# Performance work log

Hardware: AMD Instinct MI355X
Metric: run time of the kernel (lower is better)

Reference implementation:

```python
import math
import jax, jax.numpy as jnp
import numpy as np

B, IMG, CIN = 32, 32, 4
PATCH, HIDDEN, DEPTH, HEADS, MLP = 2, 768, 12, 12, 3072
FREQ, NUM_CLASSES = 256, 1000
GRID = IMG // PATCH
N = GRID * GRID
OUT = PATCH * PATCH * CIN


def _pos_embed(dim, length):
    # faithful port of get_2d_sincos_pos_embed
    g = int(math.sqrt(length))
    grid = np.stack(np.meshgrid(np.arange(g, dtype=np.float32),
                                np.arange(g, dtype=np.float32), indexing='ij')).reshape(2, -1)
    def emb1d(d, pos):
        omega = 1.0 / 10000.0 ** (np.arange(d // 2, dtype=np.float32) / (d / 2.0))
        out = np.einsum('m,d->md', pos, omega)
        return np.concatenate([np.sin(out), np.cos(out)], axis=1)
    pe = np.concatenate([emb1d(dim // 2, grid[0]), emb1d(dim // 2, grid[1])], axis=1)
    return jnp.asarray(pe[None], dtype=jnp.float32)  # [1, N, dim]


def _ln(x):
    # LayerNorm(elementwise_affine=False), eps=1e-5, biased variance
    m = jnp.mean(x, axis=-1, keepdims=True)
    v = jnp.var(x, axis=-1, keepdims=True)
    return (x - m) * jax.lax.rsqrt(v + 1e-5)


def setup_inputs() -> dict:
    key = jax.random.key(0)
    ks = jax.random.split(key, 20)
    w = lambda k, shape: jax.random.normal(k, shape, jnp.float32) * 0.02
    z = lambda *shape: jnp.zeros(shape, jnp.float32)
    return {
        'x': jax.random.normal(ks[0], (B, IMG, IMG, CIN), jnp.float32),
        't': jax.random.uniform(ks[1], (B,), jnp.float32) * 1000.0,
        'y': jax.random.randint(ks[2], (B,), 0, NUM_CLASSES + 1),
        'patch_w': w(ks[3], (PATCH * PATCH * CIN, HIDDEN)), 'patch_b': z(HIDDEN),
        't_w1': w(ks[4], (FREQ, HIDDEN)), 't_b1': z(HIDDEN),
        't_w2': w(ks[5], (HIDDEN, HIDDEN)), 't_b2': z(HIDDEN),
        'label_emb': w(ks[6], (NUM_CLASSES + 1, HIDDEN)),
        'ada_w': w(ks[7], (DEPTH, HIDDEN, 6 * HIDDEN)), 'ada_b': z(DEPTH, 6 * HIDDEN),
        'q_w': w(ks[8], (DEPTH, HIDDEN, HIDDEN)), 'q_b': z(DEPTH, HIDDEN),
        'k_w': w(ks[9], (DEPTH, HIDDEN, HIDDEN)), 'k_b': z(DEPTH, HIDDEN),
        'v_w': w(ks[10], (DEPTH, HIDDEN, HIDDEN)), 'v_b': z(DEPTH, HIDDEN),
        'o_w': w(ks[11], (DEPTH, HIDDEN, HIDDEN)), 'o_b': z(DEPTH, HIDDEN),
        'fc1_w': w(ks[12], (DEPTH, HIDDEN, MLP)), 'fc1_b': z(DEPTH, MLP),
        'fc2_w': w(ks[13], (DEPTH, MLP, HIDDEN)), 'fc2_b': z(DEPTH, HIDDEN),
        'fin_ada_w': w(ks[14], (HIDDEN, 2 * HIDDEN)), 'fin_ada_b': z(2 * HIDDEN),
        'fin_w': w(ks[15], (HIDDEN, OUT)), 'fin_b': z(OUT),
    }


def reference(x, t, y, patch_w, patch_b, t_w1, t_b1, t_w2, t_b2, label_emb,
              ada_w, ada_b, q_w, q_b, k_w, k_b, v_w, v_b, o_w, o_b,
              fc1_w, fc1_b, fc2_w, fc2_b, fin_ada_w, fin_ada_b, fin_w, fin_b):
    Bx = x.shape[0]
    dh = HIDDEN // HEADS
    # patch embed (conv k=p, stride=p == per-patch linear)
    patches = x.reshape(Bx, GRID, PATCH, GRID, PATCH, CIN)
    patches = patches.transpose(0, 1, 3, 2, 4, 5).reshape(Bx, N, PATCH * PATCH * CIN)
    h = patches @ patch_w + patch_b + _pos_embed(HIDDEN, N)
    # timestep embedding: [cos, sin] order
    half = FREQ // 2
    freqs = jnp.exp(-math.log(10000.0) * jnp.arange(half, dtype=jnp.float32) / half)
    args = t.astype(jnp.float32)[:, None] * freqs[None]
    temb = jnp.concatenate([jnp.cos(args), jnp.sin(args)], axis=-1)
    temb = jax.nn.silu(temb @ t_w1 + t_b1) @ t_w2 + t_b2
    c_act = jax.nn.silu(temb + label_emb[y])  # silu applied inside each block on c

    def block(hx, p):
        aw, ab, qw, qb, kw, kb, vw, vb, ow, ob, f1w, f1b, f2w, f2b = p
        ada = c_act @ aw + ab
        sh_m, sc_m, g_m, sh_p, sc_p, g_p = jnp.split(ada, 6, axis=-1)
        xn = _ln(hx) * (1.0 + sc_m[:, None]) + sh_m[:, None]
        q = ((xn @ qw + qb).reshape(Bx, N, HEADS, dh)) / math.sqrt(3.0)
        k = (xn @ kw + kb).reshape(Bx, N, HEADS, dh)
        v = (xn @ vw + vb).reshape(Bx, N, HEADS, dh)
        attn = jax.nn.softmax(jnp.einsum('bqhc,bkhc->bhqk', q, k).astype(jnp.float32), axis=-1)
        yv = jnp.einsum('bhqk,bkhc->bqhc', attn, v).reshape(Bx, N, HIDDEN)
        hx = hx + g_m[:, None] * (yv @ ow + ob)
        xn2 = _ln(hx) * (1.0 + sc_p[:, None]) + sh_p[:, None]
        mlp = jax.nn.gelu(xn2 @ f1w + f1b, approximate=False) @ f2w + f2b
        hx = hx + g_p[:, None] * mlp
        return hx, None

    h, _ = jax.lax.scan(block, h, (ada_w, ada_b, q_w, q_b, k_w, k_b, v_w, v_b,
                                   o_w, o_b, fc1_w, fc1_b, fc2_w, fc2_b))
    # final layer
    fada = c_act @ fin_ada_w + fin_ada_b
    sh, sc = jnp.split(fada, 2, axis=-1)
    out = (_ln(h) * (1.0 + sc[:, None]) + sh[:, None]) @ fin_w + fin_b
    return out  # [B, N, patch*patch*out_channels]
```

## Files before the change

### kernel.cpp

```cpp
#include <hip/hip_runtime.h>
#include <hip/hip_bf16.h>


typedef short  s16x8 __attribute__((ext_vector_type(8)));
typedef float  f32x4 __attribute__((ext_vector_type(4)));

__device__ __forceinline__ float bf2f(unsigned short u) {
    union { unsigned int i; float f; } v; v.i = ((unsigned int)u) << 16; return v.f;
}
__device__ __forceinline__ unsigned short f2bf(float f) {
    union { float f; unsigned int i; } v; v.f = f;
    unsigned int r = (v.i + 0x7FFFu + ((v.i >> 16) & 1u)) >> 16;
    return (unsigned short)r;
}
__device__ __forceinline__ float silu(float v) { return v / (1.f + __expf(-v)); }

__device__ __forceinline__ void gload16(const void* gptr, void* lptr) {
    __builtin_amdgcn_global_load_lds(
        (const __attribute__((address_space(1))) unsigned int*)gptr,
        (__attribute__((address_space(3))) unsigned int*)lptr,
        16, 0, 0);
}

#define ROWS 8192
#define HID  768
#define MLPD 3072
#define ADA_LD 4608

__global__ __launch_bounds__(256) void ada_init(const float* __restrict__ ada_b,
                                                const float* __restrict__ fada_b,
                                                const float* __restrict__ t_b1,
                                                const float* __restrict__ t_b2,
                                                const float* __restrict__ lemb,
                                                const int* __restrict__ y,
                                                float* __restrict__ ada_all,
                                                float* __restrict__ fada,
                                                float* __restrict__ z1,
                                                float* __restrict__ z2)
{
    const int bid = blockIdx.x, tid = threadIdx.x;
    if (bid >= 222) {
        const int col = (bid - 222) * 256 + tid;
        const float b1v = t_b1[col], b2v = t_b2[col];
        for (int r = 0; r < 32; ++r) {
            z1[(size_t)r * HID + col] = b1v;
            z2[(size_t)r * HID + col] = b2v + lemb[(size_t)y[r] * HID + col];
        }
        return;
    }
    const float* Bv; float* Out; int ldw, colb;
    if (bid < 216) {
        const int l = bid / 18; colb = (bid % 18) * 256;
        Bv = ada_b + (size_t)l * ADA_LD; Out = ada_all + (size_t)l * 32 * ADA_LD; ldw = ADA_LD;
    } else {
        colb = (bid - 216) * 256;
        Bv = fada_b; Out = fada; ldw = 1536;
    }
    const int col = colb + tid;
    const float bb = Bv[col];
    #pragma unroll
    for (int r = 0; r < 32; ++r) Out[(size_t)r * ldw + col] = bb;
}

__global__ __launch_bounds__(256) void temb1_k(const float* __restrict__ t,
                                               const float* __restrict__ w1,
                                               float* __restrict__ z1)
{
    __shared__ float tin[128];
    const int b = blockIdx.x, cc = blockIdx.y, kc = blockIdx.z, tid = threadIdx.x;
    const int k0 = kc * 128;
    if (tid < 128) {
        const int k = k0 + tid, j = k & 127;
        const float fr = __expf((float)j * (-9.210340371976184f / 128.f));
        const float a = t[b] * fr;
        tin[tid] = (k < 128) ? cosf(a) : sinf(a);
    }
    __syncthreads();
    const int col = cc * 256 + tid;
    float acc = 0.f;
    #pragma unroll 8
    for (int kk = 0; kk < 128; ++kk) acc += tin[kk] * w1[(size_t)(k0 + kk) * HID + col];
    atomicAdd(&z1[(size_t)b * HID + col], acc);
}

__global__ __launch_bounds__(256) void temb2_k(const float* __restrict__ z1,
                                               const float* __restrict__ w2,
                                               float* __restrict__ z2)
{
    __shared__ float tin[192];
    const int b = blockIdx.x, cc = blockIdx.y, kc = blockIdx.z, tid = threadIdx.x;
    const int k0 = kc * 192;
    if (tid < 192) tin[tid] = silu(z1[(size_t)b * HID + k0 + tid]);
    __syncthreads();
    const int col = cc * 256 + tid;
    float acc = 0.f;
    #pragma unroll 8
    for (int kk = 0; kk < 192; ++kk) acc += tin[kk] * w2[(size_t)(k0 + kk) * HID + col];
    atomicAdd(&z2[(size_t)b * HID + col], acc);
}

__global__ __launch_bounds__(256) void ada_gemm2(const float* __restrict__ z2,
                                                 const float* __restrict__ ada_w,
                                                 const float* __restrict__ fada_w,
                                                 float* __restrict__ ada_all,
                                                 float* __restrict__ fada)
{
    const int bx = blockIdx.x, kc = blockIdx.y, tid = threadIdx.x;
    const float* W; float* Out; int ldw, colb;
    if (bx < 216) {
        const int l = bx / 18; colb = (bx % 18) * 256;
        W = ada_w + (size_t)l * HID * ADA_LD; Out = ada_all + (size_t)l * 32 * ADA_LD; ldw = ADA_LD;
    } else {
        colb = (bx - 216) * 256;
        W = fada_w; Out = fada; ldw = 1536;
    }
    const int col = colb + tid;
    const int k0 = kc * 96;
    __shared__ float cs_[32][96];
    for (int i = tid; i < 32 * 96; i += 256)
        cs_[i / 96][i % 96] = silu(z2[(size_t)(i / 96) * HID + k0 + (i % 96)]);
    __syncthreads();
    float acc[32];
    #pragma unroll
    for (int r = 0; r < 32; ++r) acc[r] = 0.f;
    #pragma unroll 2
    for (int kk = 0; kk < 96; kk += 4) {
        const float w0 = W[(size_t)(k0 + kk) * ldw + col];
        const float w1 = W[(size_t)(k0 + kk + 1) * ldw + col];
        const float w2 = W[(size_t)(k0 + kk + 2) * ldw + col];
        const float w3 = W[(size_t)(k0 + kk + 3) * ldw + col];
        #pragma unroll
        for (int r = 0; r < 32; ++r) {
            const float4 cv = *(const float4*)&cs_[r][kk];
            acc[r] += cv.x * w0 + cv.y * w1 + cv.z * w2 + cv.w * w3;
        }
    }
    #pragma unroll
    for (int r = 0; r < 32; ++r) atomicAdd(&Out[(size_t)r * ldw + col], acc[r]);
}

__global__ __launch_bounds__(256) void patch_embed(const float* __restrict__ x,
                                                   const float* __restrict__ pw,
                                                   const float* __restrict__ pb,
                                                   float* __restrict__ h)
{
    const int row = blockIdx.x;
    const int b = row >> 8, n = row & 255;
    const int gi = n >> 4, gj = n & 15;
    const int tid = threadIdx.x;
    __shared__ float pv[16];
    if (tid < 16) {
        const int pr = tid >> 3, pc = (tid >> 2) & 1, ci = tid & 3;
        pv[tid] = x[((size_t)(b * 32 + gi * 2 + pr) * 32 + (gj * 2 + pc)) * 4 + ci];
    }
    __syncthreads();
    #pragma unroll
    for (int cc = 0; cc < 3; ++cc) {
        const int col = cc * 256 + tid;
        float acc = pb[col];
        #pragma unroll
        for (int i = 0; i < 16; ++i) acc += pv[i] * pw[(size_t)i * HID + col];
        const int d4 = (col < 384) ? col : col - 384;
        const int pos = (col < 384) ? gi : gj;
        const float kf = (float)(d4 < 192 ? d4 : d4 - 192);
        const float om = __expf(kf * (-9.210340371976184f / 192.f));
        const float a = (float)pos * om;
        acc += (d4 < 192) ? sinf(a) : cosf(a);
        h[(size_t)row * HID + col] = acc;
    }
}

__global__ __launch_bounds__(256) void convert_weights(
    const float* __restrict__ q_w, const float* __restrict__ k_w,
    const float* __restrict__ v_w, const float* __restrict__ o_w,
    const float* __restrict__ fc1_w, const float* __restrict__ fc2_w,
    const float* __restrict__ q_b, const float* __restrict__ k_b,
    const float* __restrict__ v_b,
    unsigned short* __restrict__ wbase, size_t slot_stride,
    float* __restrict__ cbias, int first_layer)
{
    const int bid = blockIdx.x;
    const int l = first_layer + bid / 6913;
    const int t = bid % 6913;
    unsigned short* dst = wbase + (size_t)(bid / 6913) * slot_stride;
    const int tid = threadIdx.x;
    if (t == 6912) {
        float* cb = cbias + (size_t)l * 2304;
        for (int i = tid; i < 2304; i += 256) {
            float v;
            if (i < 768)       v = q_b[(size_t)l * 768 + i];
            else if (i < 1536) v = k_b[(size_t)l * 768 + i - 768];
            else               v = v_b[(size_t)l * 768 + i - 1536];
            cb[i] = v;
        }
        return;
    }
    const float* src; int srcN; unsigned short* d; int dLd; int tr, tc;
    if (t < 2304) {
        const int mat = t / 576, tt = t % 576; tr = tt / 24; tc = tt % 24;
        srcN = 768; dLd = 768;
        if (mat == 0)      { src = q_w + (size_t)l * 589824; d = dst; }
        else if (mat == 1) { src = k_w + (size_t)l * 589824; d = dst + 589824; }
        else if (mat == 2) { src = v_w + (size_t)l * 589824; d = dst + 1179648; }
        else               { src = o_w + (size_t)l * 589824; d = dst + 1769472; }
    } else if (t < 4608) {
        const int tt = t - 2304; tr = tt / 96; tc = tt % 96;
        src = fc1_w + (size_t)l * 2359296; srcN = 3072; dLd = 768; d = dst + 2359296;
    } else {
        const int tt = t - 4608; tr = tt / 24; tc = tt % 24;
        src = fc2_w + (size_t)l * 2359296; srcN = 768; dLd = 3072; d = dst + 4718592;
    }
    __shared__ float lt[32][33];
    const int tx = tid & 31, ty = tid >> 5;
    const int r0 = tr * 32, c0 = tc * 32;
    #pragma unroll
    for (int i = 0; i < 4; ++i)
        lt[ty + i * 8][tx] = src[(size_t)(r0 + ty + i * 8) * srcN + c0 + tx];
    __syncthreads();
    const int q = tid & 15;
    const int cw = tid >> 4;
    #pragma unroll
    for (int i = 0; i < 2; ++i) {
        const int cc = cw + i * 16;
        const unsigned int pk = (unsigned int)f2bf(lt[2 * q][cc])
                              | ((unsigned int)f2bf(lt[2 * q + 1][cc]) << 16);
        *(unsigned int*)&d[(size_t)(c0 + cc) * dLd + r0 + 2 * q] = pk;
    }
}

__global__ __launch_bounds__(192) void ln_mod(const float* __restrict__ hbuf,
                                              const float* __restrict__ mod,
                                              int sh_off, int sc_off, int mld,
                                              unsigned short* __restrict__ xout)
{
    const int row = blockIdx.x, tid = threadIdx.x;
    const float4 xv = *(const float4*)&hbuf[(size_t)row * HID + tid * 4];
    float s = (xv.x + xv.y) + (xv.z + xv.w);
    float ss = (xv.x * xv.x + xv.y * xv.y) + (xv.z * xv.z + xv.w * xv.w);
    #pragma unroll
    for (int d = 1; d < 64; d <<= 1) { s += __shfl_xor(s, d); ss += __shfl_xor(ss, d); }
    __shared__ float sb[3], ssb[3];
    if ((tid & 63) == 0) { sb[tid >> 6] = s; ssb[tid >> 6] = ss; }
    __syncthreads();
    s = sb[0] + sb[1] + sb[2];
    ss = ssb[0] + ssb[1] + ssb[2];
    const float mean = s * (1.f / 768.f);
    const float var = ss * (1.f / 768.f) - mean * mean;
    const float rs = rsqrtf(var + 1e-5f);
    const int b = row >> 8;
    const float* mrow = mod + (size_t)b * mld;
    const float4 sc = *(const float4*)&mrow[sc_off + tid * 4];
    const float4 sh = *(const float4*)&mrow[sh_off + tid * 4];
    ushort4 o;
    o.x = f2bf((xv.x - mean) * rs * (1.f + sc.x) + sh.x);
    o.y = f2bf((xv.y - mean) * rs * (1.f + sc.y) + sh.y);
    o.z = f2bf((xv.z - mean) * rs * (1.f + sc.z) + sh.z);
    o.w = f2bf((xv.w - mean) * rs * (1.f + sc.w) + sh.w);
    *(ushort4*)&xout[(size_t)row * HID + tid * 4] = o;
}

template<int EPI, int BN>
__global__ __launch_bounds__(256) void gemm_bt(const unsigned short* __restrict__ A,
                                               const unsigned short* __restrict__ Bt,
                                               const float* __restrict__ bias,
                                               void* __restrict__ outp,
                                               const float* __restrict__ gate,
                                               int K, int ldo)
{
    constexpr int BELEMS = BN * 32;
    constexpr int NJ = BN / 32;
    __shared__ unsigned short sAB[2][4096 + BELEMS];
    const int tid = threadIdx.x;
    const int lane = tid & 63;
    const int w = tid >> 6;
    const int wm = w >> 1, wn = w & 1;
    const int nwg = gridDim.x * gridDim.y;
    int bidl = blockIdx.y * gridDim.x + blockIdx.x;
    bidl = (bidl & 7) * (nwg >> 3) + (bidl >> 3);
    const int bx = bidl % gridDim.x, by = bidl / gridDim.x;
    const int rowbase = by << 7;
    const int colbase = bx * BN;
    const size_t a0 = (size_t)(rowbase +      (tid >> 2)) * K + (tid & 3) * 8;
    const size_t a1 = (size_t)(rowbase + 64 + (tid >> 2)) * K + (tid & 3) * 8;
    const size_t b0 = (size_t)(colbase +      (tid >> 2)) * K + (tid & 3) * 8;
    size_t b1 = 0;
    if constexpr (BN == 128)
        b1 = (size_t)(colbase + 64 + (tid >> 2)) * K + (tid & 3) * 8;
    const int ldsw = w * 512;
    f32x4 acc[4][NJ];
    #pragma unroll
    for (int i = 0; i < 4; ++i)
        #pragma unroll
        for (int j = 0; j < NJ; ++j) acc[i][j] = (f32x4){0.f, 0.f, 0.f, 0.f};
    const int nk = K >> 5;
    const int lm = lane & 15, lg = lane >> 4;
    {
        unsigned short* base = &sAB[0][0];
        gload16(A + a0,  base + ldsw);
        gload16(A + a1,  base + 2048 + ldsw);
        gload16(Bt + b0, base + 4096 + ldsw);
        if constexpr (BN == 128) gload16(Bt + b1, base + 6144 + ldsw);
    }
    __syncthreads();
    int cur = 0;
    for (int kt = 0; kt < nk; ++kt) {
        if (kt + 1 < nk) {
            const int k0 = (kt + 1) << 5;
            unsigned short* base = &sAB[cur ^ 1][0];
            gload16(A + a0 + k0,  base + ldsw);
            gload16(A + a1 + k0,  base + 2048 + ldsw);
            gload16(Bt + b0 + k0, base + 4096 + ldsw);
            if constexpr (BN == 128) gload16(Bt + b1 + k0, base + 6144 + ldsw);
        }
        const unsigned short* sAc = &sAB[cur][0];
        const unsigned short* sBc = &sAB[cur][4096];
        s16x8 af[4], bfr[NJ];
        #pragma unroll
        for (int mi = 0; mi < 4; ++mi)
            af[mi] = *(const s16x8*)&sAc[(wm * 64 + mi * 16 + lm) * 32 + lg * 8];
        #pragma unroll
        for (int nj = 0; nj < NJ; ++nj)
            bfr[nj] = *(const s16x8*)&sBc[(wn * (16 * NJ) + nj * 16 + lm) * 32 + lg * 8];
        #pragma unroll
        for (int mi = 0; mi < 4; ++mi)
            #pragma unroll
            for (int nj = 0; nj < NJ; ++nj)
                acc[mi][nj] = __builtin_amdgcn_mfma_f32_16x16x32_bf16(af[mi], bfr[nj], acc[mi][nj], 0, 0, 0);
        __syncthreads();
        cur ^= 1;
    }
    float bv[NJ], gv[NJ];
    #pragma unroll
    for (int nj = 0; nj < NJ; ++nj) {
        const int col = colbase + wn * (16 * NJ) + nj * 16 + lm;
        bv[nj] = bias[col];
        if constexpr (EPI == 2) gv[nj] = gate[(size_t)(rowbase >> 8) * ADA_LD + col];
    }
    #pragma unroll
    for (int mi = 0; mi < 4; ++mi) {
        const int row = rowbase + wm * 64 + mi * 16 + (lg << 2);
        #pragma unroll
        for (int nj = 0; nj < NJ; ++nj) {
            const int col = colbase + wn * (16 * NJ) + nj * 16 + lm;
            #pragma unroll
            for (int r = 0; r < 4; ++r) {
                const float v = acc[mi][nj][r] + bv[nj];
                if constexpr (EPI == 0) {
                    ((unsigned short*)outp)[(size_t)(row + r) * ldo + col] = f2bf(v);
                } else if constexpr (EPI == 1) {
                    const float g = 0.5f * v * (1.f + erff(v * 0.70710678118654752f));
                    ((unsigned short*)outp)[(size_t)(row + r) * ldo + col] = f2bf(g);
                } else {
                    float* O = (float*)outp;
                    const size_t idx = (size_t)(row + r) * ldo + col;
                    O[idx] = O[idx] + gv[nj] * v;
                }
            }
        }
    }
}

__global__ __launch_bounds__(256) void attn_fused(const unsigned short* __restrict__ qkv,
                                                  unsigned short* __restrict__ yv)
{
    __shared__ unsigned short Vt[64][264];
    __shared__ unsigned short Psm[4][32 * 72];
    __shared__ float Ssc[4][32];
    const int bid = blockIdx.x;
    const int b = bid / 24, rem = bid % 24, h = rem >> 1, half = rem & 1;
    const int tid = threadIdx.x, w = tid >> 6, lane = tid & 63;
    {
        const int dhg = tid & 7, tk = tid >> 3;
        #pragma unroll
        for (int g = 0; g < 8; ++g) {
            const int tok = tk + g * 32;
            s16x8 vv = *(const s16x8*)(qkv + (size_t)(b * 256 + tok) * 2304 + 1536 + h * 64 + dhg * 8);
            #pragma unroll
            for (int j = 0; j < 8; ++j) Vt[dhg * 8 + j][tok] = (unsigned short)vv[j];
        }
    }
    __syncthreads();
    const int q0 = half * 128 + w * 32;
    const int lm = lane & 15, lg = lane >> 4;
    const unsigned short* Qb = qkv + (size_t)(b * 256 + q0) * 2304 + h * 64;
    s16x8 qf[2][2];
    #pragma unroll
    for (int ni = 0; ni < 2; ++ni)
        #pragma unroll
        for (int kk = 0; kk < 2; ++kk)
            qf[ni][kk] = *(const s16x8*)(Qb + (size_t)(ni * 16 + lm) * 2304 + kk * 32 + lg * 8);
    f32x4 o_[2][4];
    #pragma unroll
    for (int i = 0; i < 2; ++i)
        #pragma unroll
        for (int j = 0; j < 4; ++j) o_[i][j] = (f32x4){0.f, 0.f, 0.f, 0.f};
    float m_[2], l_[2];
    #pragma unroll
    for (int i = 0; i < 2; ++i) { m_[i] = -1e30f; l_[i] = 0.f; }
    const float s3 = 0.57735026918962576f;
    for (int c = 0; c < 4; ++c) {
        f32x4 st[4][2];
        #pragma unroll
        for (int i = 0; i < 4; ++i)
            #pragma unroll
            for (int j = 0; j < 2; ++j) st[i][j] = (f32x4){0.f, 0.f, 0.f, 0.f};
        const unsigned short* Kb = qkv + (size_t)(b * 256 + c * 64) * 2304 + 768 + h * 64;
        __builtin_amdgcn_s_setprio(1);
        #pragma unroll
        for (int kk = 0; kk < 2; ++kk)
            #pragma unroll
            for (int mi = 0; mi < 4; ++mi) {
                const s16x8 kf = *(const s16x8*)(Kb + (size_t)(mi * 16 + lm) * 2304 + kk * 32 + lg * 8);
                #pragma unroll
                for (int ni = 0; ni < 2; ++ni)
                    st[mi][ni] = __builtin_amdgcn_mfma_f32_16x16x32_bf16(kf, qf[ni][kk], st[mi][ni], 0, 0, 0);
            }
        __builtin_amdgcn_s_setprio(0);
        #pragma unroll
        for (int ni = 0; ni < 2; ++ni) {
            float cm = -1e30f;
            #pragma unroll
            for (int mi = 0; mi < 4; ++mi)
                #pragma unroll
                for (int r = 0; r < 4; ++r) cm = fmaxf(cm, st[mi][ni][r]);
            cm = fmaxf(cm, __shfl_xor(cm, 16));
            cm = fmaxf(cm, __shfl_xor(cm, 32));
            cm *= s3;
            const float mn = fmaxf(m_[ni], cm);
            const float corr = __expf(m_[ni] - mn);
            float cs = 0.f;
            #pragma unroll
            for (int mi = 0; mi < 4; ++mi) {
                float p0 = __expf(st[mi][ni][0] * s3 - mn);
                float p1 = __expf(st[mi][ni][1] * s3 - mn);
                float p2 = __expf(st[mi][ni][2] * s3 - mn);
                float p3 = __expf(st[mi][ni][3] * s3 - mn);
                cs += (p0 + p1) + (p2 + p3);
                uint2 pk;
                pk.x = (unsigned int)f2bf(p0) | ((unsigned int)f2bf(p1) << 16);
                pk.y = (unsigned int)f2bf(p2) | ((unsigned int)f2bf(p3) << 16);
                *(uint2*)&Psm[w][(ni * 16 + lm) * 72 + mi * 16 + lg * 4] = pk;
            }
            cs += __shfl_xor(cs, 16);
            cs += __shfl_xor(cs, 32);
            l_[ni] = l_[ni] * corr + cs;
            m_[ni] = mn;
            if (lane < 16) Ssc[w][ni * 16 + lane] = corr;
        }
        asm volatile("" ::: "memory");
        #pragma unroll
        for (int qi = 0; qi < 2; ++qi) {
            float fr[4];
            #pragma unroll
            for (int r = 0; r < 4; ++r) fr[r] = Ssc[w][qi * 16 + lg * 4 + r];
            #pragma unroll
            for (int di = 0; di < 4; ++di)
                #pragma unroll
                for (int r = 0; r < 4; ++r) o_[qi][di][r] *= fr[r];
        }
        __builtin_amdgcn_s_setprio(1);
        #pragma unroll
        for (int kk = 0; kk < 2; ++kk)
            #pragma unroll
            for (int qi = 0; qi < 2; ++qi) {
                const s16x8 pa = *(const s16x8*)&Psm[w][(qi * 16 + lm) * 72 + kk * 32 + lg * 8];
                #pragma unroll
                for (int di = 0; di < 4; ++di) {
                    const s16x8 vb = *(const s16x8*)&Vt[di * 16 + lm][c * 64 + kk * 32 + lg * 8];
                    o_[qi][di] = __builtin_amdgcn_mfma_f32_16x16x32_bf16(pa, vb, o_[qi][di], 0, 0, 0);
                }
            }
        __builtin_amdgcn_s_setprio(0);
    }
    asm volatile("" ::: "memory");
    if (lane < 16) {
        #pragma unroll
        for (int ni = 0; ni < 2; ++ni) Ssc[w][ni * 16 + lane] = 1.f / l_[ni];
    }
    asm volatile("" ::: "memory");
    #pragma unroll
    for (int qi = 0; qi < 2; ++qi) {
        float fr[4];
        #pragma unroll
        for (int r = 0; r < 4; ++r) fr[r] = Ssc[w][qi * 16 + lg * 4 + r];
        #pragma unroll
        for (int di = 0; di < 4; ++di)
            #pragma unroll
            for (int r = 0; r < 4; ++r) {
                const float val = o_[qi][di][r] * fr[r];
                yv[(size_t)(b * 256 + q0 + qi * 16 + lg * 4 + r) * HID + h * 64 + di * 16 + lm] = f2bf(val);
            }
    }
}

__global__ __launch_bounds__(256) void fin_gemm(const unsigned short* __restrict__ xn,
                                                const float* __restrict__ w,
                                                const float* __restrict__ bias,
                                                float* __restrict__ out)
{
    __shared__ unsigned short xs[16 * 768];
    const int rb = blockIdx.x * 16, tid = threadIdx.x;
    #pragma unroll
    for (int i = 0; i < 6; ++i) {
        const int v = tid + i * 256;
        const int row = v / 96, koff = (v % 96) * 8;
        *(s16x8*)&xs[v * 8] = *(const s16x8*)(xn + (size_t)(rb + row) * HID + koff);
    }
    __syncthreads();
    const int r = tid >> 4, o = tid & 15;
    float acc = bias[o];
    #pragma unroll 8
    for (int k = 0; k < 768; ++k) acc += bf2f(xs[r * 768 + k]) * w[(size_t)k * 16 + o];
    out[(size_t)(rb + r) * 16 + o] = acc;
}

extern "C" void kernel_launch(void* const* d_in, const int* in_sizes, int n_in,
                              void* d_out, int out_size, void* d_ws, size_t ws_size,
                              hipStream_t stream)
{
    const float* x        = (const float*)d_in[0];
    const float* t        = (const float*)d_in[1];
    const int*   y        = (const int*)d_in[2];
    const float* patch_w  = (const float*)d_in[3];
    const float* patch_b  = (const float*)d_in[4];
    const float* t_w1     = (const float*)d_in[5];
    const float* t_b1     = (const float*)d_in[6];
    const float* t_w2     = (const float*)d_in[7];
    const float* t_b2     = (const float*)d_in[8];
    const float* label_e  = (const float*)d_in[9];
    const float* ada_w    = (const float*)d_in[10];
    const float* ada_b    = (const float*)d_in[11];
    const float* q_w      = (const float*)d_in[12];
    const float* q_b      = (const float*)d_in[13];
    const float* k_w      = (const float*)d_in[14];
    const float* k_b      = (const float*)d_in[15];
    const float* v_w      = (const float*)d_in[16];
    const float* v_b      = (const float*)d_in[17];
    const float* o_w      = (const float*)d_in[18];
    const float* o_b      = (const float*)d_in[19];
    const float* fc1_w    = (const float*)d_in[20];
    const float* fc1_b    = (const float*)d_in[21];
    const float* fc2_w    = (const float*)d_in[22];
    const float* fc2_b    = (const float*)d_in[23];
    const float* fada_w   = (const float*)d_in[24];
    const float* fada_b   = (const float*)d_in[25];
    const float* fin_w    = (const float*)d_in[26];
    const float* fin_b    = (const float*)d_in[27];

    char* ws = (char*)d_ws;
    size_t off = 0;
    auto alloc = [&](size_t bytes) { size_t o = off; off = (off + bytes + 255) & ~(size_t)255; return o; };
    const size_t OFF_H    = alloc((size_t)ROWS * HID * 4);
    const size_t OFF_XN   = alloc((size_t)ROWS * HID * 2);
    const size_t OFF_QKV  = alloc((size_t)ROWS * 2304 * 2);
    const size_t OFF_YV   = alloc((size_t)ROWS * HID * 2);
    const size_t OFF_MLP  = alloc((size_t)ROWS * MLPD * 2);
    const size_t OFF_ADA  = alloc((size_t)12 * 32 * ADA_LD * 4);
    const size_t OFF_FADA = alloc((size_t)32 * 1536 * 4);
    const size_t OFF_Z2   = alloc((size_t)32 * HID * 4);
    const size_t OFF_Z1   = alloc((size_t)32 * HID * 4);
    const size_t OFF_CB   = alloc((size_t)12 * 2304 * 4);
    const size_t OFF_W    = off;
    const size_t WSLOT_ELEMS = 7077888;
    const bool big = (ws_size >= OFF_W + (size_t)12 * WSLOT_ELEMS * 2);

    float*          h     = (float*)(ws + OFF_H);
    unsigned short* xn    = (unsigned short*)(ws + OFF_XN);
    unsigned short* qkv   = (unsigned short*)(ws + OFF_QKV);
    unsigned short* yv    = (unsigned short*)(ws + OFF_YV);
    unsigned short* mlp   = (unsigned short*)(ws + OFF_MLP);
    float*          adaA  = (float*)(ws + OFF_ADA);
    float*          fada  = (float*)(ws + OFF_FADA);
    float*          z2    = (float*)(ws + OFF_Z2);
    float*          z1    = (float*)(ws + OFF_Z1);
    float*          cbias = (float*)(ws + OFF_CB);
    unsigned short* wsW   = (unsigned short*)(ws + OFF_W);

    ada_init<<<225, 256, 0, stream>>>(ada_b, fada_b, t_b1, t_b2, label_e, y,
                                      adaA, fada, z1, z2);
    temb1_k<<<dim3(32, 3, 2), 256, 0, stream>>>(t, t_w1, z1);
    temb2_k<<<dim3(32, 3, 4), 256, 0, stream>>>(z1, t_w2, z2);
    ada_gemm2<<<dim3(222, 8), 256, 0, stream>>>(z2, ada_w, fada_w, adaA, fada);
    patch_embed<<<8192, 256, 0, stream>>>(x, patch_w, patch_b, h);
    if (big) {
        convert_weights<<<6913 * 12, 256, 0, stream>>>(q_w, k_w, v_w, o_w, fc1_w, fc2_w,
                                                       q_b, k_b, v_b, wsW, WSLOT_ELEMS, cbias, 0);
    }

    for (int l = 0; l < 12; ++l) {
        unsigned short* wslot = wsW + (big ? (size_t)l * WSLOT_ELEMS : 0);
        if (!big) {
            convert_weights<<<6913, 256, 0, stream>>>(q_w, k_w, v_w, o_w, fc1_w, fc2_w,
                                                      q_b, k_b, v_b, wslot, 0, cbias, l);
        }
        unsigned short* qkvT = wslot;
        unsigned short* oT   = wslot + 1769472;
        unsigned short* f1T  = wslot + 2359296;
        unsigned short* f2T  = wslot + 4718592;
        float* ada_l  = adaA + (size_t)l * 32 * ADA_LD;
        float* cb_l   = cbias + (size_t)l * 2304;

        ln_mod<<<8192, 192, 0, stream>>>(h, ada_l, 0, 768, ADA_LD, xn);
        gemm_bt<0, 128><<<dim3(18, 64), 256, 0, stream>>>(xn, qkvT, cb_l, qkv, nullptr, 768, 2304);
        attn_fused<<<768, 256, 0, stream>>>(qkv, yv);
        gemm_bt<2, 64><<<dim3(12, 64), 256, 0, stream>>>(yv, oT, o_b + (size_t)l * 768, h,
                                                         ada_l + 1536, 768, 768);
        ln_mod<<<8192, 192, 0, stream>>>(h, ada_l, 2304, 3072, ADA_LD, xn);
        gemm_bt<1, 128><<<dim3(24, 64), 256, 0, stream>>>(xn, f1T, fc1_b + (size_t)l * 3072, mlp,
                                                          nullptr, 768, 3072);
        gemm_bt<2, 64><<<dim3(12, 64), 256, 0, stream>>>(mlp, f2T, fc2_b + (size_t)l * 768, h,
                                                         ada_l + 3840, 3072, 768);
    }

    ln_mod<<<8192, 192, 0, stream>>>(h, fada, 0, 768, 1536, xn);
    fin_gemm<<<512, 256, 0, stream>>>(xn, fin_w, fin_b, (float*)d_out);
}
```

Baseline: 3.414 ms.

## Compute adaLN modulation GEMM with bf16 MFMA on pre-transposed weights

Adds kernels that transpose and convert the adaLN and final-adaLN weights to bf16, apply SiLU to the conditioning vector in bf16, and run the modulation GEMM with MFMA instructions using double-buffered LDS staging. This replaces the fp32 CUDA-core GEMM that relied on atomic adds over K-chunks. It adds an extra full pass over the fp32 weights to convert them, plus extra workspace, and it lowers precision of the modulation outputs to bf16 inputs.

```diff
diff --git a/kernel.cpp b/kernel.cpp
--- a/kernel.cpp
+++ b/kernel.cpp
@@ -99,6 +99,15 @@
     atomicAdd(&z2[(size_t)b * HID + col], acc);
 }
 
+__global__ __launch_bounds__(256) void csilu_k(const float* __restrict__ z2,
+                                               unsigned short* __restrict__ cact_bf)
+{
+    const int base = (blockIdx.x * 256 + threadIdx.x) * 8;
+    #pragma unroll
+    for (int i = 0; i < 8; ++i)
+        cact_bf[base + i] = f2bf(silu(z2[base + i]));
+}
+
 __global__ __launch_bounds__(256) void ada_gemm2(const float* __restrict__ z2,
                                                  const float* __restrict__ ada_w,
                                                  const float* __restrict__ fada_w,
@@ -137,6 +146,76 @@
     }
     #pragma unroll
     for (int r = 0; r < 32; ++r) atomicAdd(&Out[(size_t)r * ldw + col], acc[r]);
+}
+
+__global__ __launch_bounds__(256) void ada_mfma(const unsigned short* __restrict__ cact_bf,
+                                                const unsigned short* __restrict__ adaT,
+                                                const unsigned short* __restrict__ fadaT,
+                                                const float* __restrict__ ada_b,
+                                                const float* __restrict__ fada_b,
+                                                float* __restrict__ ada_all,
+                                                float* __restrict__ fada)
+{
+    __shared__ unsigned short sB[2][8192];
+    const int bx = blockIdx.x, tid = threadIdx.x;
+    const unsigned short* Bt; const float* bias; float* Out; int ldw, colb;
+    if (bx < 216) {
+        const int l = bx / 18; colb = (bx % 18) * 256;
+        Bt = adaT + (size_t)l * ADA_LD * HID;
+        bias = ada_b + (size_t)l * ADA_LD;
+        Out = ada_all + (size_t)l * 32 * ADA_LD; ldw = ADA_LD;
+    } else {
+        colb = (bx - 216) * 256;
+        Bt = fadaT; bias = fada_b; Out = fada; ldw = 1536;
+    }
+    const int lane = tid & 63, w = tid >> 6;
+    const int lm = lane & 15, lg = lane >> 4;
+    auto stageB = [&](int buf, int kt) {
+        #pragma unroll
+        for (int g = 0; g < 4; ++g) {
+            const int gi = g * 256 + tid;
+            const int col = gi >> 2, k8 = (gi & 3) * 8;
+            gload16(Bt + (size_t)(colb + col) * HID + kt * 32 + k8,
+                    &sB[buf][0] + (size_t)gi * 8);
+        }
+    };
+    f32x4 acc[2][4];
+    #pragma unroll
+    for (int i = 0; i < 2; ++i)
+        #pragma unroll
+        for (int j = 0; j < 4; ++j) acc[i][j] = (f32x4){0.f, 0.f, 0.f, 0.f};
+    stageB(0, 0);
+    __syncthreads();
+    int cur = 0;
+    for (int kt = 0; kt < 24; ++kt) {
+        if (kt + 1 < 24) stageB(cur ^ 1, kt + 1);
+        s16x8 af[2], bfr[4];
+        #pragma unroll
+        for (int mi = 0; mi < 2; ++mi)
+            af[mi] = *(const s16x8*)(cact_bf + (size_t)(mi * 16 + lm) * HID + kt * 32 + lg * 8);
+        #pragma unroll
+        for (int nj = 0; nj < 4; ++nj)
+            bfr[nj] = *(const s16x8*)&sB[cur][(w * 64 + nj * 16 + lm) * 32 + lg * 8];
+        #pragma unroll
+        for (int mi = 0; mi < 2; ++mi)
+            #pragma unroll
+            for (int nj = 0; nj < 4; ++nj)
+                acc[mi][nj] = __builtin_amdgcn_mfma_f32_16x16x32_bf16(af[mi], bfr[nj], acc[mi][nj], 0, 0, 0);
+        __syncthreads();
+        cur ^= 1;
+    }
+    #pragma unroll
+    for (int mi = 0; mi < 2; ++mi) {
+        const int row = mi * 16 + (lg << 2);
+        #pragma unroll
+        for (int nj = 0; nj < 4; ++nj) {
+            const int col = colb + w * 64 + nj * 16 + lm;
+            const float bb = bias[col];
+            #pragma unroll
+            for (int r = 0; r < 4; ++r)
+                Out[(size_t)(row + r) * ldw + col] = acc[mi][nj][r] + bb;
+        }
+    }
 }
 
 __global__ __launch_bounds__(256) void patch_embed(const float* __restrict__ x,
@@ -225,6 +304,40 @@
         const unsigned int pk = (unsigned int)f2bf(lt[2 * q][cc])
                               | ((unsigned int)f2bf(lt[2 * q + 1][cc]) << 16);
         *(unsigned int*)&d[(size_t)(c0 + cc) * dLd + r0 + 2 * q] = pk;
+    }
+}
+
+__global__ __launch_bounds__(256) void convert_ada(
+    const float* __restrict__ ada_w, const float* __restrict__ fada_w,
+    unsigned short* __restrict__ adaT, unsigned short* __restrict__ fadaT)
+{
+    const int bid = blockIdx.x, tid = threadIdx.x;
+    const float* src; unsigned short* d; int srcN, tr, tc;
+    if (bid < 41472) {
+        const int l = bid / 3456, tt = bid % 3456;
+        tr = tt / 144; tc = tt % 144;
+        src = ada_w + (size_t)l * HID * ADA_LD; srcN = ADA_LD;
+        d = adaT + (size_t)l * ADA_LD * HID;
+    } else {
+        const int tt = bid - 41472;
+        tr = tt / 48; tc = tt % 48;
+        src = fada_w; srcN = 1536; d = fadaT;
+    }
+    __shared__ float lt[32][33];
+    const int tx = tid & 31, ty = tid >> 5;
+    const int r0 = tr * 32, c0 = tc * 32;
+    #pragma unroll
+    for (int i = 0; i < 4; ++i)
+        lt[ty + i * 8][tx] = src[(size_t)(r0 + ty + i * 8) * srcN + c0 + tx];
+    __syncthreads();
+    const int q = tid & 15;
+    const int cw = tid >> 4;
+    #pragma unroll
+    for (int i = 0; i < 2; ++i) {
+        const int cc = cw + i * 16;
+        const unsigned int pk = (unsigned int)f2bf(lt[2 * q][cc])
+                              | ((unsigned int)f2bf(lt[2 * q + 1][cc]) << 16);
+        *(unsigned int*)&d[(size_t)(c0 + cc) * HID + r0 + 2 * q] = pk;
     }
 }
 
@@ -550,17 +663,20 @@
     char* ws = (char*)d_ws;
     size_t off = 0;
     auto alloc = [&](size_t bytes) { size_t o = off; off = (off + bytes + 255) & ~(size_t)255; return o; };
-    const size_t OFF_H    = alloc((size_t)ROWS * HID * 4);
-    const size_t OFF_XN   = alloc((size_t)ROWS * HID * 2);
-    const size_t OFF_QKV  = alloc((size_t)ROWS * 2304 * 2);
-    const size_t OFF_YV   = alloc((size_t)ROWS * HID * 2);
-    const size_t OFF_MLP  = alloc((size_t)ROWS * MLPD * 2);
-    const size_t OFF_ADA  = alloc((size_t)12 * 32 * ADA_LD * 4);
-    const size_t OFF_FADA = alloc((size_t)32 * 1536 * 4);
-    const size_t OFF_Z2   = alloc((size_t)32 * HID * 4);
-    const size_t OFF_Z1   = alloc((size_t)32 * HID * 4);
-    const size_t OFF_CB   = alloc((size_t)12 * 2304 * 4);
-    const size_t OFF_W    = off;
+    const size_t OFF_H     = alloc((size_t)ROWS * HID * 4);
+    const size_t OFF_XN    = alloc((size_t)ROWS * HID * 2);
+    const size_t OFF_QKV   = alloc((size_t)ROWS * 2304 * 2);
+    const size_t OFF_YV    = alloc((size_t)ROWS * HID * 2);
+    const size_t OFF_MLP   = alloc((size_t)ROWS * MLPD * 2);
+    const size_t OFF_ADA   = alloc((size_t)12 * 32 * ADA_LD * 4);
+    const size_t OFF_FADA  = alloc((size_t)32 * 1536 * 4);
+    const size_t OFF_Z2    = alloc((size_t)32 * HID * 4);
+    const size_t OFF_Z1    = alloc((size_t)32 * HID * 4);
+    const size_t OFF_CB    = alloc((size_t)12 * 2304 * 4);
+    const size_t OFF_CBF   = alloc((size_t)32 * HID * 2);
+    const size_t OFF_ADAT  = alloc((size_t)12 * ADA_LD * HID * 2);
+    const size_t OFF_FADAT = alloc((size_t)1536 * HID * 2);
+    const size_t OFF_W     = off;
     const size_t WSLOT_ELEMS = 7077888;
     const bool big = (ws_size >= OFF_W + (size_t)12 * WSLOT_ELEMS * 2);
 
@@ -574,18 +690,25 @@
     float*          z2    = (float*)(ws + OFF_Z2);
     float*          z1    = (float*)(ws + OFF_Z1);
     float*          cbias = (float*)(ws + OFF_CB);
+    unsigned short* cactb = (unsigned short*)(ws + OFF_CBF);
+    unsigned short* adaT  = (unsigned short*)(ws + OFF_ADAT);
+    unsigned short* fadaT = (unsigned short*)(ws + OFF_FADAT);
     unsigned short* wsW   = (unsigned short*)(ws + OFF_W);
 
     ada_init<<<225, 256, 0, stream>>>(ada_b, fada_b, t_b1, t_b2, label_e, y,
                                       adaA, fada, z1, z2);
     temb1_k<<<dim3(32, 3, 2), 256, 0, stream>>>(t, t_w1, z1);
     temb2_k<<<dim3(32, 3, 4), 256, 0, stream>>>(z1, t_w2, z2);
-    ada_gemm2<<<dim3(222, 8), 256, 0, stream>>>(z2, ada_w, fada_w, adaA, fada);
-    patch_embed<<<8192, 256, 0, stream>>>(x, patch_w, patch_b, h);
     if (big) {
+        convert_ada<<<42624, 256, 0, stream>>>(ada_w, fada_w, adaT, fadaT);
+        csilu_k<<<12, 256, 0, stream>>>(z2, cactb);
+        ada_mfma<<<222, 256, 0, stream>>>(cactb, adaT, fadaT, ada_b, fada_b, adaA, fada);
         convert_weights<<<6913 * 12, 256, 0, stream>>>(q_w, k_w, v_w, o_w, fc1_w, fc2_w,
                                                        q_b, k_b, v_b, wsW, WSLOT_ELEMS, cbias, 0);
-    }
+    } else {
+        ada_gemm2<<<dim3(222, 8), 256, 0, stream>>>(z2, ada_w, fada_w, adaA, fada);
+    }
+    patch_embed<<<8192, 256, 0, stream>>>(x, patch_w, patch_b, h);
 
     for (int l = 0; l < 12; ++l) {
         unsigned short* wslot = wsW + (big ? (size_t)l * WSLOT_ELEMS : 0);
```

After: 3.404 ms. About the same (-0.3%).
